# Kernel tuning notes

Hardware: AMD Instinct MI355X
Metric: run time of the kernel (lower is better)

## Reference

```python
import jax, jax.numpy as jnp
import numpy as np

N_VOCAB = 50400
D_MODEL = 4096
SHARDS = 8  # cores_per_replica; psum over shards sums each shard's bias


def setup_inputs() -> dict:
    key = jax.random.key(0)
    k_x, k_w, k_b = jax.random.split(key, 3)
    x = jax.random.randint(k_x, (2, 2048), 0, N_VOCAB, dtype=jnp.int64)
    # hk.Linear per shard: W_s is [in_dim_per_shard, d_model]; concatenated over
    # shards this is the full [n_vocab, d_model] table. TruncatedNormal(1/sqrt(n_vocab)).
    W = jax.random.truncated_normal(k_w, -2.0, 2.0, (N_VOCAB, D_MODEL), dtype=jnp.float32) / np.sqrt(N_VOCAB).astype(np.float32)
    # one bias per shard (hk.Linear zero-init by default; use small random for a
    # nontrivial reference); psum sums all shard biases.
    b = jax.random.normal(k_b, (SHARDS, D_MODEL), dtype=jnp.float32) * 0.02
    return {"x": x, "W": W, "b": b}


def reference(x, W, b):
    # Original: each shard builds a one-hot [tokens, in_dim_per_shard] vs its
    # vocab slice, matmuls against its W slice, adds its bias, then psums over
    # shards. Mathematically: full one-hot matmul + sum of shard biases.
    tok = x.reshape(-1)                                   # [T]
    onehot = jax.nn.one_hot(tok, N_VOCAB, dtype=jnp.float32)  # [T, V] (the wasteful dense trick)
    out = jnp.einsum('tv,vd->td', onehot, W) + b.sum(axis=0)  # [T, D]
    return out
```

## Files before the change

### kernel.cpp

```cpp
#include <hip/hip_runtime.h>
#include <hip/hip_bf16.h>

#define D_MODEL 4096
#define SHARDS 8

__global__ __launch_bounds__(256) void bias_sum_kernel(const float* __restrict__ b,
                                                       float* __restrict__ bsum) {
    int d = blockIdx.x * blockDim.x + threadIdx.x;
    const float4* b4 = (const float4*)b;
    float4 acc = b4[d];
#pragma unroll
    for (int s = 1; s < SHARDS; ++s) {
        float4 v = b4[s * (D_MODEL / 4) + d];
        acc.x += v.x; acc.y += v.y; acc.z += v.z; acc.w += v.w;
    }
    ((float4*)bsum)[d] = acc;
}

__global__ __launch_bounds__(256) void gather_bias_kernel(const int* __restrict__ tok,
                                                          const float* __restrict__ W,
                                                          const float* __restrict__ bsum,
                                                          float* __restrict__ out) {
    const int t = blockIdx.x;
    const int row = tok[t];
    const float4* __restrict__ Wrow = (const float4*)(W + (long long)row * D_MODEL);
    const float4* __restrict__ bs4  = (const float4*)bsum;
    float4* __restrict__ out4       = (float4*)(out + (long long)t * D_MODEL);
    const int tid = threadIdx.x;
#pragma unroll
    for (int i = 0; i < 4; ++i) {
        const int idx = tid + i * 256;
        float4 w = Wrow[idx];
        const float4 bb = bs4[idx];
        w.x += bb.x; w.y += bb.y; w.z += bb.z; w.w += bb.w;
        out4[idx] = w;
    }
}

extern "C" void kernel_launch(void* const* d_in, const int* in_sizes, int n_in,
                              void* d_out, int out_size, void* d_ws, size_t ws_size,
                              hipStream_t stream) {
    const int*   tok = (const int*)d_in[0];
    const float* W   = (const float*)d_in[1];
    const float* b   = (const float*)d_in[2];
    float* out  = (float*)d_out;
    float* bsum = (float*)d_ws;

    const int T = in_sizes[0];

    bias_sum_kernel<<<(D_MODEL / 4) / 256, 256, 0, stream>>>(b, bsum);
    gather_bias_kernel<<<T, 256, 0, stream>>>(tok, W, bsum, out);
}
```

Before: 901.0 us.

## Fuse bias-sum into gather kernel and process four tokens per block

Merges the separate bias reduction kernel into the embedding gather kernel. Each block now recomputes the summed bias in registers and reuses it across four tokens, reading the token ids with a single vector load. This removes one kernel launch and the workspace round trip. In exchange, every block re-reads the 8x4096 bias array (which should mostly hit cache), and the grid shrinks to a quarter of the previous block count.

```diff
diff --git a/kernel.cpp b/kernel.cpp
--- a/kernel.cpp
+++ b/kernel.cpp
@@ -3,37 +3,52 @@
 
 #define D_MODEL 4096
 #define SHARDS 8
+#define TPB 4
 
-__global__ __launch_bounds__(256) void bias_sum_kernel(const float* __restrict__ b,
-                                                       float* __restrict__ bsum) {
-    int d = blockIdx.x * blockDim.x + threadIdx.x;
-    const float4* b4 = (const float4*)b;
-    float4 acc = b4[d];
+__global__ __launch_bounds__(256) void embed_fused_kernel(const int* __restrict__ tok,
+                                                          const float* __restrict__ W,
+                                                          const float* __restrict__ b,
+                                                          float* __restrict__ out,
+                                                          int T) {
+    const int tid = threadIdx.x;
+    const int t0  = blockIdx.x * TPB;
+
+    int rows[TPB];
+    if (t0 + TPB <= T) {
+        const int4 r4 = ((const int4*)tok)[blockIdx.x];
+        rows[0] = r4.x; rows[1] = r4.y; rows[2] = r4.z; rows[3] = r4.w;
+    } else {
 #pragma unroll
-    for (int s = 1; s < SHARDS; ++s) {
-        float4 v = b4[s * (D_MODEL / 4) + d];
-        acc.x += v.x; acc.y += v.y; acc.z += v.z; acc.w += v.w;
+        for (int j = 0; j < TPB; ++j) rows[j] = (t0 + j < T) ? tok[t0 + j] : 0;
     }
-    ((float4*)bsum)[d] = acc;
-}
 
-__global__ __launch_bounds__(256) void gather_bias_kernel(const int* __restrict__ tok,
-                                                          const float* __restrict__ W,
-                                                          const float* __restrict__ bsum,
-                                                          float* __restrict__ out) {
-    const int t = blockIdx.x;
-    const int row = tok[t];
-    const float4* __restrict__ Wrow = (const float4*)(W + (long long)row * D_MODEL);
-    const float4* __restrict__ bs4  = (const float4*)bsum;
-    float4* __restrict__ out4       = (float4*)(out + (long long)t * D_MODEL);
-    const int tid = threadIdx.x;
+    const float4* __restrict__ b4 = (const float4*)b;
+    float4 bb[4];
 #pragma unroll
     for (int i = 0; i < 4; ++i) {
-        const int idx = tid + i * 256;
-        float4 w = Wrow[idx];
-        const float4 bb = bs4[idx];
-        w.x += bb.x; w.y += bb.y; w.z += bb.z; w.w += bb.w;
-        out4[idx] = w;
+        const int d = tid + i * 256;
+        float4 acc = b4[d];
+#pragma unroll
+        for (int s = 1; s < SHARDS; ++s) {
+            const float4 v = b4[s * (D_MODEL / 4) + d];
+            acc.x += v.x; acc.y += v.y; acc.z += v.z; acc.w += v.w;
+        }
+        bb[i] = acc;
+    }
+
+#pragma unroll
+    for (int j = 0; j < TPB; ++j) {
+        const int t = t0 + j;
+        if (t >= T) break;
+        const float4* __restrict__ Wrow = (const float4*)(W + (long long)rows[j] * D_MODEL);
+        float4* __restrict__ out4       = (float4*)(out + (long long)t * D_MODEL);
+#pragma unroll
+        for (int i = 0; i < 4; ++i) {
+            const int idx = tid + i * 256;
+            float4 w = Wrow[idx];
+            w.x += bb[i].x; w.y += bb[i].y; w.z += bb[i].z; w.w += bb[i].w;
+            out4[idx] = w;
+        }
     }
 }
 
@@ -43,11 +58,10 @@
     const int*   tok = (const int*)d_in[0];
     const float* W   = (const float*)d_in[1];
     const float* b   = (const float*)d_in[2];
-    float* out  = (float*)d_out;
-    float* bsum = (float*)d_ws;
+    float* out = (float*)d_out;
 
     const int T = in_sizes[0];
+    const int grid = (T + TPB - 1) / TPB;
 
-    bias_sum_kernel<<<(D_MODEL / 4) / 256, 256, 0, stream>>>(b, bsum);
-    gather_bias_kernel<<<T, 256, 0, stream>>>(tok, W, bsum, out);
+    embed_fused_kernel<<<grid, 256, 0, stream>>>(tok, W, b, out, T);
 }
```

After: 899.7 us. About the same (-0.1%).
